# Kernel tuning notes

Hardware: AMD Instinct MI355X
Metric: run time of the kernel (lower is better)

Reference implementation:

```python
import jax, jax.numpy as jnp
import numpy as np

EPS = 0.3          # FAGCN eps residual coefficient
N_LAYERS = 2


def setup_inputs() -> dict:
    key = jax.random.key(0)
    ks = jax.random.split(key, 8)
    N, E, IN, H, OUT = 50000, 800000, 256, 64, 16
    return {
        "h": jax.random.normal(ks[0], (N, IN), dtype=jnp.float32),
        "src": jax.random.randint(ks[1], (E,), 0, N, dtype=jnp.int32),
        "dst": jax.random.randint(ks[2], (E,), 0, N, dtype=jnp.int32),
        "t1_w": jax.random.normal(ks[3], (H, IN), dtype=jnp.float32) * (1.414 / np.sqrt(IN)),
        "t1_b": jnp.zeros((H,), dtype=jnp.float32),
        "gate_w": jax.random.normal(ks[4], (N_LAYERS, 2 * H), dtype=jnp.float32) * (1.414 / np.sqrt(2 * H)),
        "gate_b": jnp.zeros((N_LAYERS,), dtype=jnp.float32),
        "t2_w": jax.random.normal(ks[5], (OUT, H), dtype=jnp.float32) * (1.414 / np.sqrt(H)),
        "t2_b": jnp.zeros((OUT,), dtype=jnp.float32),
    }


def reference(h, src, dst, t1_w, t1_b, gate_w, gate_b, t2_w, t2_b):
    N = h.shape[0]
    # symmetric degree norm d = in_degree^-0.5 (as in FAGCN preprocessing)
    deg = jnp.zeros((N,), dtype=h.dtype).at[dst].add(1.0)
    d = jax.lax.rsqrt(jnp.maximum(deg, 1.0))

    # t1 + relu (dropout is identity in eval mode)
    x = jax.nn.relu(h @ t1_w.T + t1_b)          # [N, H]
    raw = x
    for l in range(N_LAYERS):
        hs = x[src]                              # [E, H] gathered src feats
        hd = x[dst]                              # [E, H] gathered dst feats
        # gate(concat[dst, src]) -> tanh -> scalar per edge
        g = jnp.tanh(jnp.concatenate([hd, hs], axis=-1) @ gate_w[l] + gate_b[l])  # [E]
        e = g * d[dst] * d[src]                  # [E]
        msg = hs * e[:, None]                    # [E, H]
        z = jax.ops.segment_sum(msg, dst, num_segments=N)  # scatter-sum to dst
        x = EPS * raw + z

    logits = x @ t2_w.T + t2_b                   # [N, OUT]
    return jax.nn.log_softmax(logits, axis=-1)
```

## Files before the change

kernel.cpp:

```cpp
#include <hip/hip_runtime.h>
#include <math.h>

#define EPS 0.3f
#define CAP 64
#define SPILLCAP 65536

typedef __attribute__((ext_vector_type(8))) short bf16x8;
typedef __attribute__((ext_vector_type(4))) float f32x4;

__device__ __forceinline__ short f2bf(float f) {
    union { float f; unsigned u; } v; v.f = f;
    unsigned r = v.u + 0x7FFFu + ((v.u >> 16) & 1u);
    return (short)(r >> 16);
}
__device__ __forceinline__ float bf2f(short s) {
    union { unsigned u; float f; } v;
    v.u = ((unsigned)(unsigned short)s) << 16;
    return v.f;
}
__device__ __forceinline__ int f2bf_pk(float lo, float hi) {
#if __has_builtin(__builtin_amdgcn_cvt_pk_bf16_f32)
    auto r = __builtin_amdgcn_cvt_pk_bf16_f32(lo, hi);
    int out; __builtin_memcpy(&out, &r, 4);
    return out;
#else
    return ((int)(unsigned short)f2bf(lo)) | (((int)(unsigned short)f2bf(hi)) << 16);
#endif
}
__device__ __forceinline__ float fast_tanh(float x) {
    return 1.0f - 2.0f / (1.0f + __expf(2.0f * x));
}

__global__ __launch_bounds__(256) void init_k(const float* __restrict__ w,
                                              short* __restrict__ wb,
                                              int* __restrict__ cnt,
                                              int* __restrict__ spillN, int N) {
    int bid = blockIdx.x, tid = threadIdx.x;
    if (bid < 64) wb[bid * 256 + tid] = f2bf(w[bid * 256 + tid]);
    for (int i = bid * 256 + tid; i < N; i += gridDim.x * 256) cnt[i] = 0;
    if (bid == 0 && tid == 0) *spillN = 0;
}

#define LROW 264
__global__ __launch_bounds__(256) void scatter_t1(
    const int* __restrict__ src, const int* __restrict__ dst, int E,
    int* __restrict__ cnt, unsigned short* __restrict__ esrc2,
    unsigned* __restrict__ spill, int* __restrict__ spillN,
    const float* __restrict__ h, const short* __restrict__ wb,
    const float* __restrict__ t1b, const float* __restrict__ gw,
    short* __restrict__ XAh, float* __restrict__ ga0, float* __restrict__ gb0,
    int N, int SCB)
{
    __shared__ short lds[4][16 * LROW];
    int tid = threadIdx.x;

    if ((int)blockIdx.x < SCB) {
        for (int i = blockIdx.x * 256 + tid; i < E; i += SCB * 256) {
            int d = dst[i];
            int slot = atomicAdd(&cnt[d], 1);
            if (slot < CAP) {
                esrc2[(size_t)d * CAP + slot] = (unsigned short)src[i];
            } else {
                int sp = atomicAdd(spillN, 1);
                if (sp < SPILLCAP)
                    spill[sp] = ((unsigned)d << 16) | ((unsigned)src[i] & 0xFFFFu);
            }
        }
        return;
    }

    int bid = blockIdx.x - SCB;
    int wave = tid >> 6;
    int lane = tid & 63;
    int l15 = lane & 15, quad = lane >> 4;
    int M0 = (bid * 4 + wave) * 16;
    if (M0 >= N) return;
    int rlim = N - M0;

    short* myl = lds[wave];
    const float* hb = h + (size_t)M0 * 256;
    #pragma unroll
    for (int r = 0; r < 16; ++r) {
        if (r < rlim) {
            float4 v = *(const float4*)&hb[(size_t)r * 256 + lane * 4];
            int2 sv; sv.x = f2bf_pk(v.x, v.y); sv.y = f2bf_pk(v.z, v.w);
            *(int2*)&myl[r * LROW + lane * 4] = sv;
        }
    }

    f32x4 acc[4];
    #pragma unroll
    for (int nt = 0; nt < 4; ++nt) acc[nt] = (f32x4){0.f, 0.f, 0.f, 0.f};

    const short* wq = wb + quad * 8;
    #pragma unroll
    for (int kc = 0; kc < 256; kc += 32) {
        bf16x8 af = *(const bf16x8*)&myl[l15 * LROW + kc + quad * 8];
        #pragma unroll
        for (int nt = 0; nt < 4; ++nt) {
            bf16x8 bf = *(const bf16x8*)(wq + (size_t)(nt * 16 + l15) * 256 + kc);
            acc[nt] = __builtin_amdgcn_mfma_f32_16x16x32_bf16(af, bf, acc[nt], 0, 0, 0);
        }
    }

    float pa[4] = {0.f, 0.f, 0.f, 0.f};
    float pb[4] = {0.f, 0.f, 0.f, 0.f};
    #pragma unroll
    for (int nt = 0; nt < 4; ++nt) {
        int n = nt * 16 + l15;
        float bias = t1b[n];
        float gd = gw[n], gs = gw[64 + n];
        #pragma unroll
        for (int r = 0; r < 4; ++r) {
            int row = quad * 4 + r;
            if (row < rlim) {
                float x = fmaxf(acc[nt][r] + bias, 0.f);
                XAh[(size_t)(M0 + row) * 64 + n] = f2bf(x);
                pa[r] += x * gd;
                pb[r] += x * gs;
            }
        }
    }
    #pragma unroll
    for (int off = 1; off < 16; off <<= 1) {
        #pragma unroll
        for (int r = 0; r < 4; ++r) {
            pa[r] += __shfl_xor(pa[r], off, 64);
            pb[r] += __shfl_xor(pb[r], off, 64);
        }
    }
    if (l15 == 0) {
        #pragma unroll
        for (int r = 0; r < 4; ++r) {
            int row = quad * 4 + r;
            if (row < rlim) {
                ga0[M0 + row] = pa[r];
                gb0[M0 + row] = pb[r];
            }
        }
    }
}

__device__ __forceinline__ void gather_core5(
    const int* __restrict__ cnt, const unsigned short* __restrict__ esrc2,
    const float* __restrict__ a, const float* __restrict__ gb,
    const unsigned* __restrict__ spill, const int* __restrict__ spillN,
    const short* __restrict__ xch, const short* __restrict__ rawh,
    float gbias, int t, int lane, int N, float fin[8])
{
    int g = (lane >> 3) & 3;
    int l = lane & 7;
    int j = lane & 31;
    int hbase = lane & 32;

    int beg = t * CAP;
    int ev_raw = (int)esrc2[beg + j];
    int deg = cnt[t];
    float atg = a[t] + gbias;
    int evc = min(ev_raw, N - 1);

    int degrow = min(deg, CAP);
    int lim = min(degrow, 32);
    int lim1 = max(lim - 1, 0);

    int sarr[8];
    #pragma unroll
    for (int k = 0; k < 8; ++k) {
        int m = g + 4 * k;
        sarr[k] = __shfl(evc, hbase + min(m, lim1), 64);
    }
    bf16x8 xr[8];
    #pragma unroll
    for (int k = 0; k < 8; ++k)
        xr[k] = *(const bf16x8*)&xch[(size_t)sarr[k] * 64 + l * 8];

    float gbe = gb[evc];
    float ce  = (float)cnt[evc];
    float cv = fast_tanh(atg + gbe) * rsqrtf(fmaxf(ce, 1.0f));
    float carr[8];
    #pragma unroll
    for (int k = 0; k < 8; ++k) {
        int m = g + 4 * k;
        float c = __shfl(cv, hbase + min(m, lim1), 64);
        carr[k] = (m < lim) ? c : 0.f;
    }

    float acc[8];
    #pragma unroll
    for (int k = 0; k < 8; ++k) acc[k] = 0.f;
    #pragma unroll
    for (int k = 0; k < 8; ++k) {
        float c0 = carr[k];
        #pragma unroll
        for (int kk = 0; kk < 8; ++kk) acc[kk] += c0 * bf2f(xr[k][kk]);
    }

    for (int i = beg + 32 + g; i < beg + degrow; i += 4) {
        int s0 = (int)esrc2[i];
        float c0 = fast_tanh(atg + gb[s0]) * rsqrtf(fmaxf((float)cnt[s0], 1.f));
        bf16x8 x0 = *(const bf16x8*)&xch[(size_t)s0 * 64 + l * 8];
        #pragma unroll
        for (int k = 0; k < 8; ++k) acc[k] += c0 * bf2f(x0[k]);
    }
    int sn = min(*spillN, SPILLCAP);
    if (sn > 0) {
        for (int i = 0; i < sn; ++i) {
            unsigned e = spill[i];
            if ((int)(e >> 16) == t && g == 0) {
                int s0 = (int)(e & 0xFFFFu);
                float c0 = fast_tanh(atg + gb[s0]) * rsqrtf(fmaxf((float)cnt[s0], 1.f));
                bf16x8 x0 = *(const bf16x8*)&xch[(size_t)s0 * 64 + l * 8];
                #pragma unroll
                for (int k = 0; k < 8; ++k) acc[k] += c0 * bf2f(x0[k]);
            }
        }
    }

    #pragma unroll
    for (int off = 8; off < 32; off <<= 1) {
        #pragma unroll
        for (int k = 0; k < 8; ++k) acc[k] += __shfl_xor(acc[k], off, 64);
    }

    float dt = rsqrtf(fmaxf((float)deg, 1.0f));
    bf16x8 rv = *(const bf16x8*)&rawh[(size_t)t * 64 + l * 8];
    #pragma unroll
    for (int k = 0; k < 8; ++k) fin[k] = EPS * bf2f(rv[k]) + dt * acc[k];
}

__global__ __launch_bounds__(256) void gather_mid(
    const int* __restrict__ cnt, const unsigned short* __restrict__ esrc2,
    const float* __restrict__ a, const float* __restrict__ gb,
    const unsigned* __restrict__ spill, const int* __restrict__ spillN,
    const short* __restrict__ xch, const float* __restrict__ gbp,
    short* __restrict__ xnh, const float* __restrict__ gw_next,
    float* __restrict__ ga_next, float* __restrict__ gb_next, int N)
{
    int tid = threadIdx.x;
    int t = blockIdx.x * 8 + (tid >> 5);
    int tt = min(t, N - 1);
    bool valid = (t < N);
    int lane = tid & 63;
    int g = (lane >> 3) & 3, l = lane & 7;
    float fin[8];
    gather_core5(cnt, esrc2, a, gb, spill, spillN, xch, xch, gbp[0], tt, lane, N, fin);

    if (g == 0 && valid) {
        int4 o;
        o.x = f2bf_pk(fin[0], fin[1]); o.y = f2bf_pk(fin[2], fin[3]);
        o.z = f2bf_pk(fin[4], fin[5]); o.w = f2bf_pk(fin[6], fin[7]);
        *(int4*)&xnh[(size_t)tt * 64 + l * 8] = o;
    }
    float av = 0.f, bv = 0.f;
    #pragma unroll
    for (int k = 0; k < 8; ++k) {
        av += fin[k] * gw_next[l * 8 + k];
        bv += fin[k] * gw_next[64 + l * 8 + k];
    }
    #pragma unroll
    for (int off = 1; off < 8; off <<= 1) {
        av += __shfl_xor(av, off, 64);
        bv += __shfl_xor(bv, off, 64);
    }
    if ((lane & 31) == 0 && valid) {
        ga_next[tt] = av;
        gb_next[tt] = bv;
    }
}

__global__ __launch_bounds__(256) void gather_out(
    const int* __restrict__ cnt, const unsigned short* __restrict__ esrc2,
    const float* __restrict__ a, const float* __restrict__ gb,
    const unsigned* __restrict__ spill, const int* __restrict__ spillN,
    const short* __restrict__ xch, const short* __restrict__ rawh,
    const float* __restrict__ gbp, const float* __restrict__ t2w,
    const float* __restrict__ t2b, float* __restrict__ out, int N)
{
    int tid = threadIdx.x;
    int t = blockIdx.x * 8 + (tid >> 5);
    int tt = min(t, N - 1);
    bool valid = (t < N);
    int lane = tid & 63;
    int g = (lane >> 3) & 3, l = lane & 7;
    float fin[8];
    gather_core5(cnt, esrc2, a, gb, spill, spillN, xch, rawh, gbp[1], tt, lane, N, fin);

    int j0 = 4 * g;
    float p[4];
    #pragma unroll
    for (int i = 0; i < 4; ++i) {
        const float* w = &t2w[(size_t)(j0 + i) * 64 + l * 8];
        float s = 0.f;
        #pragma unroll
        for (int k = 0; k < 8; ++k) s += fin[k] * w[k];
        p[i] = s;
    }
    #pragma unroll
    for (int off = 1; off < 8; off <<= 1) {
        #pragma unroll
        for (int i = 0; i < 4; ++i) p[i] += __shfl_xor(p[i], off, 64);
    }
    float li[4];
    #pragma unroll
    for (int i = 0; i < 4; ++i) li[i] = p[i] + t2b[j0 + i];
    float m = fmaxf(fmaxf(li[0], li[1]), fmaxf(li[2], li[3]));
    #pragma unroll
    for (int off = 8; off < 32; off <<= 1) m = fmaxf(m, __shfl_xor(m, off, 64));
    float s = 0.f;
    #pragma unroll
    for (int i = 0; i < 4; ++i) s += __expf(li[i] - m);
    #pragma unroll
    for (int off = 8; off < 32; off <<= 1) s += __shfl_xor(s, off, 64);
    float lse = m + __logf(s);
    if (l == 0 && valid) {
        float4 o;
        o.x = li[0] - lse; o.y = li[1] - lse;
        o.z = li[2] - lse; o.w = li[3] - lse;
        *(float4*)&out[(size_t)tt * 16 + j0] = o;
    }
}

extern "C" void kernel_launch(void* const* d_in, const int* in_sizes, int n_in,
                              void* d_out, int out_size, void* d_ws, size_t ws_size,
                              hipStream_t stream) {
    const float* h    = (const float*)d_in[0];
    const int*   src  = (const int*)d_in[1];
    const int*   dst  = (const int*)d_in[2];
    const float* t1w  = (const float*)d_in[3];
    const float* t1b  = (const float*)d_in[4];
    const float* gw   = (const float*)d_in[5];
    const float* gbia = (const float*)d_in[6];
    const float* t2w  = (const float*)d_in[7];
    const float* t2b  = (const float*)d_in[8];
    float* out = (float*)d_out;

    int N = in_sizes[0] / 256;
    int E = in_sizes[1];

    char* p = (char*)d_ws;
    short*    XAh    = (short*)p;       p += (size_t)N * 64 * 2;
    short*    XBh    = (short*)p;       p += (size_t)N * 64 * 2;
    float*    ga0    = (float*)p;       p += (size_t)N * 4;
    float*    ga1    = (float*)p;       p += (size_t)N * 4;
    float*    gb0    = (float*)p;       p += (size_t)N * 4;
    float*    gb1    = (float*)p;       p += (size_t)N * 4;
    int*      cnt    = (int*)p;         p += (size_t)N * 4;
    int*      spillN = (int*)p;         p += 16;
    unsigned* spill  = (unsigned*)p;    p += (size_t)SPILLCAP * 4;
    p = (char*)(((size_t)p + 15) & ~(size_t)15);
    unsigned short* esrc2 = (unsigned short*)p; p += (size_t)N * CAP * 2;
    p = (char*)(((size_t)p + 15) & ~(size_t)15);
    short*    wbf    = (short*)p;

    init_k<<<256, 256, 0, stream>>>(t1w, wbf, cnt, spillN, N);

    int SCB = 240;
    scatter_t1<<<SCB + (N + 63) / 64, 256, 0, stream>>>(
        src, dst, E, cnt, esrc2, spill, spillN,
        h, wbf, t1b, gw, XAh, ga0, gb0, N, SCB);

    int GB = (N + 7) / 8;
    gather_mid<<<GB, 256, 0, stream>>>(cnt, esrc2, ga0, gb0, spill, spillN,
                                       XAh, gbia, XBh, gw + 128, ga1, gb1, N);
    gather_out<<<GB, 256, 0, stream>>>(cnt, esrc2, ga1, gb1, spill, spillN,
                                       XBh, XAh, gbia, t2w, t2b, out, N);
}
```

Measured before the change: 202.0 us.

## Partition edges by destination range to localize scatter atomics per XCD

Adds a pre-pass that buckets each edge chunk into 8 destination ranges in LDS and writes packed (local dst, src) words plus per-block offsets. Scatter blocks then handle only edges whose destination falls in the range picked by blockIdx mod 8, and the gather kernels map blocks to node ranges the same way. The apparent aim is to keep each range's atomics and esrc2 writes within one XCD's L2 on the MI355X. This costs an extra pass over the edge list, more workspace, and depends on the hardware assigning blocks to XCDs round-robin. It also switches some loads to nontemporal hints.

```diff
diff --git a/kernel.cpp b/kernel.cpp
--- a/kernel.cpp
+++ b/kernel.cpp
@@ -4,6 +4,8 @@
 #define EPS 0.3f
 #define CAP 64
 #define SPILLCAP 65536
+#define NR 8
+#define NPB 256
 
 typedef __attribute__((ext_vector_type(8))) short bf16x8;
 typedef __attribute__((ext_vector_type(4))) float f32x4;
@@ -31,39 +33,81 @@
     return 1.0f - 2.0f / (1.0f + __expf(2.0f * x));
 }
 
-__global__ __launch_bounds__(256) void init_k(const float* __restrict__ w,
-                                              short* __restrict__ wb,
-                                              int* __restrict__ cnt,
-                                              int* __restrict__ spillN, int N) {
-    int bid = blockIdx.x, tid = threadIdx.x;
-    if (bid < 64) wb[bid * 256 + tid] = f2bf(w[bid * 256 + tid]);
-    for (int i = bid * 256 + tid; i < N; i += gridDim.x * 256) cnt[i] = 0;
-    if (bid == 0 && tid == 0) *spillN = 0;
+__global__ __launch_bounds__(256) void part_init(
+    const int* __restrict__ src, const int* __restrict__ dst, int E,
+    const float* __restrict__ w, short* __restrict__ wb,
+    int* __restrict__ cnt, int* __restrict__ spillN,
+    unsigned* __restrict__ part2, unsigned short* __restrict__ hoff,
+    int N, int RSZ, int CS)
+{
+    extern __shared__ unsigned sbuf[];
+    __shared__ int lh[NR], lsc[NR + 1], lcur[NR];
+    int b = blockIdx.x, tid = threadIdx.x;
+    if (b < 64) wb[b * 256 + tid] = f2bf(w[b * 256 + tid]);
+    for (int i = b * 256 + tid; i < N; i += NPB * 256) cnt[i] = 0;
+    if (b == 0 && tid == 0) *spillN = 0;
+
+    int e0 = b * CS, e1 = min(e0 + CS, E);
+    if (tid < NR) lh[tid] = 0;
+    __syncthreads();
+    for (int i = e0 + tid; i < e1; i += 256)
+        atomicAdd(&lh[(unsigned)dst[i] / (unsigned)RSZ], 1);
+    __syncthreads();
+    if (tid == 0) {
+        int s = 0;
+        #pragma unroll
+        for (int r = 0; r < NR; ++r) { lsc[r] = s; s += lh[r]; }
+        lsc[NR] = s;
+    }
+    __syncthreads();
+    if (tid < NR) lcur[tid] = lsc[tid];
+    __syncthreads();
+    for (int i = e0 + tid; i < e1; i += 256) {
+        int d = dst[i];
+        int r = (unsigned)d / (unsigned)RSZ;
+        int slot = atomicAdd(&lcur[r], 1);
+        sbuf[slot] = ((unsigned)(d - r * RSZ) << 16) | ((unsigned)src[i] & 0xFFFFu);
+    }
+    __syncthreads();
+    int tot = e1 - e0;
+    for (int i = tid; i < tot; i += 256)
+        part2[(size_t)b * CS + i] = sbuf[i];
+    if (tid < NR + 1) hoff[b * (NR + 1) + tid] = (unsigned short)lsc[tid];
 }
 
 #define LROW 264
 __global__ __launch_bounds__(256) void scatter_t1(
-    const int* __restrict__ src, const int* __restrict__ dst, int E,
+    const unsigned* __restrict__ part2, const unsigned short* __restrict__ hoff,
     int* __restrict__ cnt, unsigned short* __restrict__ esrc2,
     unsigned* __restrict__ spill, int* __restrict__ spillN,
     const float* __restrict__ h, const short* __restrict__ wb,
     const float* __restrict__ t1b, const float* __restrict__ gw,
     short* __restrict__ XAh, float* __restrict__ ga0, float* __restrict__ gb0,
-    int N, int SCB)
+    int N, int SCB, int RSZ, int CS)
 {
     __shared__ short lds[4][16 * LROW];
     int tid = threadIdx.x;
 
     if ((int)blockIdx.x < SCB) {
-        for (int i = blockIdx.x * 256 + tid; i < E; i += SCB * 256) {
-            int d = dst[i];
-            int slot = atomicAdd(&cnt[d], 1);
-            if (slot < CAP) {
-                esrc2[(size_t)d * CAP + slot] = (unsigned short)src[i];
-            } else {
-                int sp = atomicAdd(spillN, 1);
-                if (sp < SPILLCAP)
-                    spill[sp] = ((unsigned)d << 16) | ((unsigned)src[i] & 0xFFFFu);
+        int x = blockIdx.x & (NR - 1);
+        int rank = blockIdx.x >> 3;
+        int nb = SCB >> 3;
+        int lo = x * RSZ;
+        for (int b = rank; b < NPB; b += nb) {
+            int o0 = hoff[b * (NR + 1) + x];
+            int o1 = hoff[b * (NR + 1) + x + 1];
+            const unsigned* seg = part2 + (size_t)b * CS;
+            for (int i = o0 + tid; i < o1; i += 256) {
+                unsigned e = __builtin_nontemporal_load(&seg[i]);
+                int d = lo + (int)(e >> 16);
+                int slot = atomicAdd(&cnt[d], 1);
+                if (slot < CAP) {
+                    esrc2[(size_t)d * CAP + slot] = (unsigned short)(e & 0xFFFFu);
+                } else {
+                    int sp = atomicAdd(spillN, 1);
+                    if (sp < SPILLCAP)
+                        spill[sp] = ((unsigned)d << 16) | (e & 0xFFFFu);
+                }
             }
         }
         return;
@@ -154,7 +198,7 @@
     int hbase = lane & 32;
 
     int beg = t * CAP;
-    int ev_raw = (int)esrc2[beg + j];
+    int ev_raw = (int)__builtin_nontemporal_load(&esrc2[beg + j]);
     int deg = cnt[t];
     float atg = a[t] + gbias;
     int evc = min(ev_raw, N - 1);
@@ -228,18 +272,28 @@
     for (int k = 0; k < 8; ++k) fin[k] = EPS * bf2f(rv[k]) + dt * acc[k];
 }
 
+__device__ __forceinline__ void node_map(int bid, int tid, int N, int RSZ,
+                                         int& t, int& tt, bool& valid) {
+    int x = bid & (NR - 1);
+    int q = bid >> 3;
+    int ln = q * 8 + (tid >> 5);
+    t = x * RSZ + ln;
+    int hi = min(x * RSZ + RSZ, N);
+    valid = (t < hi);
+    tt = valid ? t : max(hi - 1, 0);
+}
+
 __global__ __launch_bounds__(256) void gather_mid(
     const int* __restrict__ cnt, const unsigned short* __restrict__ esrc2,
     const float* __restrict__ a, const float* __restrict__ gb,
     const unsigned* __restrict__ spill, const int* __restrict__ spillN,
     const short* __restrict__ xch, const float* __restrict__ gbp,
     short* __restrict__ xnh, const float* __restrict__ gw_next,
-    float* __restrict__ ga_next, float* __restrict__ gb_next, int N)
+    float* __restrict__ ga_next, float* __restrict__ gb_next, int N, int RSZ)
 {
     int tid = threadIdx.x;
-    int t = blockIdx.x * 8 + (tid >> 5);
-    int tt = min(t, N - 1);
-    bool valid = (t < N);
+    int t, tt; bool valid;
+    node_map(blockIdx.x, tid, N, RSZ, t, tt, valid);
     int lane = tid & 63;
     int g = (lane >> 3) & 3, l = lane & 7;
     float fin[8];
@@ -274,12 +328,11 @@
     const unsigned* __restrict__ spill, const int* __restrict__ spillN,
     const short* __restrict__ xch, const short* __restrict__ rawh,
     const float* __restrict__ gbp, const float* __restrict__ t2w,
-    const float* __restrict__ t2b, float* __restrict__ out, int N)
+    const float* __restrict__ t2b, float* __restrict__ out, int N, int RSZ)
 {
     int tid = threadIdx.x;
-    int t = blockIdx.x * 8 + (tid >> 5);
-    int tt = min(t, N - 1);
-    bool valid = (t < N);
+    int t, tt; bool valid;
+    node_map(blockIdx.x, tid, N, RSZ, t, tt, valid);
     int lane = tid & 63;
     int g = (lane >> 3) & 3, l = lane & 7;
     float fin[8];
@@ -336,6 +389,8 @@
 
     int N = in_sizes[0] / 256;
     int E = in_sizes[1];
+    int RSZ = (N + NR - 1) / NR;
+    int CS  = (E + NPB - 1) / NPB;
 
     char* p = (char*)d_ws;
     short*    XAh    = (short*)p;       p += (size_t)N * 64 * 2;
@@ -350,18 +405,23 @@
     p = (char*)(((size_t)p + 15) & ~(size_t)15);
     unsigned short* esrc2 = (unsigned short*)p; p += (size_t)N * CAP * 2;
     p = (char*)(((size_t)p + 15) & ~(size_t)15);
+    unsigned* part2  = (unsigned*)p;    p += (size_t)NPB * CS * 4;
+    unsigned short* hoff = (unsigned short*)p; p += (size_t)NPB * (NR + 1) * 2;
+    p = (char*)(((size_t)p + 15) & ~(size_t)15);
     short*    wbf    = (short*)p;
 
-    init_k<<<256, 256, 0, stream>>>(t1w, wbf, cnt, spillN, N);
+    part_init<<<NPB, 256, (size_t)CS * 4, stream>>>(
+        src, dst, E, t1w, wbf, cnt, spillN, part2, hoff, N, RSZ, CS);
 
     int SCB = 240;
     scatter_t1<<<SCB + (N + 63) / 64, 256, 0, stream>>>(
-        src, dst, E, cnt, esrc2, spill, spillN,
-        h, wbf, t1b, gw, XAh, ga0, gb0, N, SCB);
-
-    int GB = (N + 7) / 8;
-    gather_mid<<<GB, 256, 0, stream>>>(cnt, esrc2, ga0, gb0, spill, spillN,
-                                       XAh, gbia, XBh, gw + 128, ga1, gb1, N);
-    gather_out<<<GB, 256, 0, stream>>>(cnt, esrc2, ga1, gb1, spill, spillN,
-                                       XBh, XAh, gbia, t2w, t2b, out, N);
-}
+        part2, hoff, cnt, esrc2, spill, spillN,
+        h, wbf, t1b, gw, XAh, ga0, gb0, N, SCB, RSZ, CS);
+
+    int PB = (RSZ + 7) / 8;
+    gather_mid<<<NR * PB, 256, 0, stream>>>(cnt, esrc2, ga0, gb0, spill, spillN,
+                                            XAh, gbia, XBh, gw + 128, ga1, gb1,
+                                            N, RSZ);
+    gather_out<<<NR * PB, 256, 0, stream>>>(cnt, esrc2, ga1, gb1, spill, spillN,
+                                            XBh, XAh, gbia, t2w, t2b, out, N, RSZ);
+}
```

New measurement: 204.0 us. Within noise of the previous version (+1.0%).

## Replace global-atomic edge bucketing with two-pass LDS partition by destination bin

Applied to the files above, without the earlier changes.

Edge bucketing used to run one global atomicAdd per edge on the per-node counters. It now runs in two passes. First, each block takes a chunk of edges, builds a local histogram by dst>>8, and writes the packed edges out grouped by bin. Then one block per 256-node bin reads its pieces from every chunk, assigns slots with LDS atomics, and writes the counts directly, so the separate zeroing pass is gone. Gather loads of the edge lists are also marked nontemporal; the cost is an extra intermediate buffer and a serial per-thread read loop in the bin blocks.

```diff
diff --git a/kernel.cpp b/kernel.cpp
--- a/kernel.cpp
+++ b/kernel.cpp
@@ -4,6 +4,7 @@
 #define EPS 0.3f
 #define CAP 64
 #define SPILLCAP 65536
+#define NPB 256
 
 typedef __attribute__((ext_vector_type(8))) short bf16x8;
 typedef __attribute__((ext_vector_type(4))) float f32x4;
@@ -31,45 +32,91 @@
     return 1.0f - 2.0f / (1.0f + __expf(2.0f * x));
 }
 
-__global__ __launch_bounds__(256) void init_k(const float* __restrict__ w,
-                                              short* __restrict__ wb,
-                                              int* __restrict__ cnt,
-                                              int* __restrict__ spillN, int N) {
-    int bid = blockIdx.x, tid = threadIdx.x;
-    if (bid < 64) wb[bid * 256 + tid] = f2bf(w[bid * 256 + tid]);
-    for (int i = bid * 256 + tid; i < N; i += gridDim.x * 256) cnt[i] = 0;
-    if (bid == 0 && tid == 0) *spillN = 0;
+__global__ __launch_bounds__(256) void part_init(
+    const int* __restrict__ src, const int* __restrict__ dst, int E,
+    const float* __restrict__ w, short* __restrict__ wb,
+    int* __restrict__ spillN,
+    unsigned* __restrict__ part2, unsigned short* __restrict__ hoff2, int CS)
+{
+    extern __shared__ unsigned sbuf[];
+    __shared__ int lh[256], tmp[256], lcur[256];
+    int b = blockIdx.x, tid = threadIdx.x;
+    if (b < 64) wb[b * 256 + tid] = f2bf(w[b * 256 + tid]);
+    if (b == 0 && tid == 0) *spillN = 0;
+
+    int e0 = b * CS, e1 = min(e0 + CS, E);
+    lh[tid] = 0;
+    __syncthreads();
+    for (int i = e0 + tid; i < e1; i += 256)
+        atomicAdd(&lh[dst[i] >> 8], 1);
+    __syncthreads();
+    int v = lh[tid];
+    tmp[tid] = v;
+    __syncthreads();
+    #pragma unroll
+    for (int off = 1; off < 256; off <<= 1) {
+        int o = (tid >= off) ? tmp[tid - off] : 0;
+        __syncthreads();
+        tmp[tid] += o;
+        __syncthreads();
+    }
+    int excl = tmp[tid] - v;
+    lcur[tid] = excl;
+    hoff2[b * 257 + tid] = (unsigned short)excl;
+    if (tid == 255) hoff2[b * 257 + 256] = (unsigned short)tmp[255];
+    __syncthreads();
+    for (int i = e0 + tid; i < e1; i += 256) {
+        int d = dst[i];
+        int slot = atomicAdd(&lcur[d >> 8], 1);
+        sbuf[slot] = ((unsigned)(d & 255) << 16) | ((unsigned)src[i] & 0xFFFFu);
+    }
+    __syncthreads();
+    int tot = e1 - e0;
+    for (int i = tid; i < tot; i += 256)
+        part2[(size_t)b * CS + i] = sbuf[i];
 }
 
 #define LROW 264
-__global__ __launch_bounds__(256) void scatter_t1(
-    const int* __restrict__ src, const int* __restrict__ dst, int E,
+__global__ __launch_bounds__(256) void bins_t1(
+    const unsigned* __restrict__ part2, const unsigned short* __restrict__ hoff2,
     int* __restrict__ cnt, unsigned short* __restrict__ esrc2,
     unsigned* __restrict__ spill, int* __restrict__ spillN,
     const float* __restrict__ h, const short* __restrict__ wb,
     const float* __restrict__ t1b, const float* __restrict__ gw,
     short* __restrict__ XAh, float* __restrict__ ga0, float* __restrict__ gb0,
-    int N, int SCB)
+    int N, int NBINS, int CS)
 {
     __shared__ short lds[4][16 * LROW];
     int tid = threadIdx.x;
 
-    if ((int)blockIdx.x < SCB) {
-        for (int i = blockIdx.x * 256 + tid; i < E; i += SCB * 256) {
-            int d = dst[i];
-            int slot = atomicAdd(&cnt[d], 1);
+    if ((int)blockIdx.x < NBINS) {
+        int b = blockIdx.x;
+        int t0 = b << 8;
+        int* lcur = (int*)&lds[0][0];
+        lcur[tid] = 0;
+        __syncthreads();
+        int o0 = hoff2[tid * 257 + b];
+        int o1 = hoff2[tid * 257 + b + 1];
+        const unsigned* seg = part2 + (size_t)tid * CS;
+        for (int i = o0; i < o1; ++i) {
+            unsigned e = __builtin_nontemporal_load(&seg[i]);
+            int dl = (int)(e >> 16);
+            int slot = atomicAdd(&lcur[dl], 1);
             if (slot < CAP) {
-                esrc2[(size_t)d * CAP + slot] = (unsigned short)src[i];
+                esrc2[(size_t)(t0 + dl) * CAP + slot] = (unsigned short)(e & 0xFFFFu);
             } else {
                 int sp = atomicAdd(spillN, 1);
                 if (sp < SPILLCAP)
-                    spill[sp] = ((unsigned)d << 16) | ((unsigned)src[i] & 0xFFFFu);
+                    spill[sp] = ((unsigned)(t0 + dl) << 16) | (e & 0xFFFFu);
             }
         }
+        __syncthreads();
+        int t = t0 + tid;
+        if (t < N) cnt[t] = lcur[tid];
         return;
     }
 
-    int bid = blockIdx.x - SCB;
+    int bid = blockIdx.x - NBINS;
     int wave = tid >> 6;
     int lane = tid & 63;
     int l15 = lane & 15, quad = lane >> 4;
@@ -154,7 +201,7 @@
     int hbase = lane & 32;
 
     int beg = t * CAP;
-    int ev_raw = (int)esrc2[beg + j];
+    int ev_raw = (int)__builtin_nontemporal_load(&esrc2[beg + j]);
     int deg = cnt[t];
     float atg = a[t] + gbias;
     int evc = min(ev_raw, N - 1);
@@ -336,6 +383,8 @@
 
     int N = in_sizes[0] / 256;
     int E = in_sizes[1];
+    int CS = (E + NPB - 1) / NPB;
+    int NBINS = (N + 255) / 256;
 
     char* p = (char*)d_ws;
     short*    XAh    = (short*)p;       p += (size_t)N * 64 * 2;
@@ -350,14 +399,17 @@
     p = (char*)(((size_t)p + 15) & ~(size_t)15);
     unsigned short* esrc2 = (unsigned short*)p; p += (size_t)N * CAP * 2;
     p = (char*)(((size_t)p + 15) & ~(size_t)15);
+    unsigned* part2  = (unsigned*)p;    p += (size_t)NPB * CS * 4;
+    unsigned short* hoff2 = (unsigned short*)p; p += (size_t)NPB * 257 * 2;
+    p = (char*)(((size_t)p + 15) & ~(size_t)15);
     short*    wbf    = (short*)p;
 
-    init_k<<<256, 256, 0, stream>>>(t1w, wbf, cnt, spillN, N);
-
-    int SCB = 240;
-    scatter_t1<<<SCB + (N + 63) / 64, 256, 0, stream>>>(
-        src, dst, E, cnt, esrc2, spill, spillN,
-        h, wbf, t1b, gw, XAh, ga0, gb0, N, SCB);
+    part_init<<<NPB, 256, (size_t)CS * 4, stream>>>(
+        src, dst, E, t1w, wbf, spillN, part2, hoff2, CS);
+
+    bins_t1<<<NBINS + (N + 63) / 64, 256, 0, stream>>>(
+        part2, hoff2, cnt, esrc2, spill, spillN,
+        h, wbf, t1b, gw, XAh, ga0, gb0, N, NBINS, CS);
 
     int GB = (N + 7) / 8;
     gather_mid<<<GB, 256, 0, stream>>>(cnt, esrc2, ga0, gb0, spill, spillN,
```

Result: faster. 196.9 us (-2.5%).
